# Kernel tuning notes

Measured on AMD Instinct MI355X. Metric: run time of the kernel, lower is better.

The kernel has to match this reference:

```python
import jax, jax.numpy as jnp
import numpy as np

N = 50000      # nodes
E = 800000     # edges (avg degree 16)
DIN = 256      # in_dim
EDIM = 16      # raw edge feature dim
H = 2          # heads
C = 64         # out_dim per head
NEG_SLOPE = 0.2


def setup_inputs() -> dict:
    key = jax.random.key(0)
    ks = jax.random.split(key, 10)
    s = 0.05
    return {
        "x": jax.random.normal(ks[0], (N, DIN), jnp.float32),
        "edge_index": jax.random.randint(ks[1], (2, E), 0, N, dtype=jnp.int64),
        "edge_attr": jax.random.normal(ks[2], (E, EDIM), jnp.float32),
        "W_ep": jax.random.normal(ks[3], (EDIM, DIN), jnp.float32) * s,
        "b_ep": jnp.zeros((DIN,), jnp.float32),
        "W_l": jax.random.normal(ks[4], (DIN, H * C), jnp.float32) * s,
        "b_l": jnp.zeros((H * C,), jnp.float32),
        "W_r": jax.random.normal(ks[5], (DIN, H * C), jnp.float32) * s,
        "b_r": jnp.zeros((H * C,), jnp.float32),
        "W_e": jax.random.normal(ks[6], (DIN, H * C), jnp.float32) * s,
        "att": jax.random.normal(ks[7], (H, C), jnp.float32) * s,
        "bias": jnp.zeros((H * C,), jnp.float32),
    }


def reference(x, edge_index, edge_attr, W_ep, b_ep, W_l, b_l, W_r, b_r, W_e, att, bias):
    src, dst = edge_index[0], edge_index[1]
    # edge_proj: Linear(edge_dim, in_dim)
    ea = edge_attr @ W_ep + b_ep                       # [E, DIN]
    # GATv2 node projections (lin_l -> source/message, lin_r -> target)
    xl = (x @ W_l + b_l).reshape(N, H, C)              # [N, H, C]
    xr = (x @ W_r + b_r).reshape(N, H, C)              # [N, H, C]
    ee = (ea @ W_e).reshape(E, H, C)                   # [E, H, C] (lin_edge, no bias)
    # per-edge combined features
    m = xl[src] + xr[dst] + ee                         # [E, H, C]
    # GATv2 attention score: att . LeakyReLU(m)
    s = jnp.einsum("ehc,hc->eh", jax.nn.leaky_relu(m, NEG_SLOPE), att)  # [E, H]
    # segment softmax over incoming edges of each target node
    smax = jax.ops.segment_max(s, dst, num_segments=N)  # [N, H]
    ex = jnp.exp(s - smax[dst])                         # [E, H]
    denom = jax.ops.segment_sum(ex, dst, num_segments=N)
    alpha = ex / denom[dst]                             # [E, H]
    # weighted scatter-add of source messages (xl[src])
    out = jax.ops.segment_sum(alpha[:, :, None] * xl[src], dst, num_segments=N)  # [N, H, C]
    return out.reshape(N, H * C) + bias
```

## Files before the change

### kernel.cpp

```cpp
#include <hip/hip_runtime.h>
#include <hip/hip_bf16.h>
#include <math.h>

#define DIN 256
#define EDIM 16
#define HC 128
#define GBM 64
#define GBN 256
#define GBK 32
#define LDS_STRIDE 40
#define BSTRIDE 64

typedef __attribute__((ext_vector_type(8))) short short8v;
typedef __attribute__((ext_vector_type(4))) float floatx4;
typedef __attribute__((ext_vector_type(2))) float floatx2;
typedef __attribute__((ext_vector_type(4))) unsigned short ushort4v;
typedef __attribute__((ext_vector_type(2))) int intx2;

__device__ inline unsigned short f2bf(float f) {
    union { float f; unsigned u; } v; v.f = f;
    unsigned r = v.u + 0x7FFF + ((v.u >> 16) & 1);
    return (unsigned short)(r >> 16);
}

__device__ inline float rsum32(float v) {
    int x;
    x = __builtin_amdgcn_update_dpp(0, __builtin_bit_cast(int, v), 0xB1, 0xF, 0xF, true);
    v += __builtin_bit_cast(float, x);
    x = __builtin_amdgcn_update_dpp(0, __builtin_bit_cast(int, v), 0x4E, 0xF, 0xF, true);
    v += __builtin_bit_cast(float, x);
    x = __builtin_amdgcn_update_dpp(0, __builtin_bit_cast(int, v), 0x124, 0xF, 0xF, true);
    v += __builtin_bit_cast(float, x);
    x = __builtin_amdgcn_update_dpp(0, __builtin_bit_cast(int, v), 0x128, 0xF, 0xF, true);
    v += __builtin_bit_cast(float, x);
    v += __builtin_bit_cast(float, __builtin_amdgcn_ds_swizzle(__builtin_bit_cast(int, v), 0x401F));
    return v;
}

__global__ void k_prep(const float* __restrict__ W_ep, const float* __restrict__ b_ep,
                       const float* __restrict__ W_e,
                       float* __restrict__ Wc, float* __restrict__ bc) {
    int tid = blockIdx.x * blockDim.x + threadIdx.x;
    if (tid < EDIM * HC) {
        int k = tid >> 7, j = tid & 127;
        float s = 0.f;
        for (int d = 0; d < DIN; ++d) s += W_ep[k * DIN + d] * W_e[d * HC + j];
        Wc[tid] = s;
    } else if (tid < EDIM * HC + HC) {
        int j = tid - EDIM * HC;
        float s = 0.f;
        for (int d = 0; d < DIN; ++d) s += b_ep[d] * W_e[d * HC + j];
        bc[j] = s;
    }
}

__global__ __launch_bounds__(256) void k_convw(const float* __restrict__ Wl,
                                               const float* __restrict__ Wr,
                                               unsigned short* __restrict__ Wb) {
    __shared__ unsigned short tile[32][33];
    int tx = threadIdx.x & 31, ty = threadIdx.x >> 5;
    int c0 = blockIdx.x * 32, k0 = blockIdx.y * 32;
#pragma unroll
    for (int i = 0; i < 4; ++i) {
        int k = k0 + ty + i * 8;
        int col = c0 + tx;
        float v = (col < HC) ? Wl[(size_t)k * HC + col] : Wr[(size_t)k * HC + (col - HC)];
        tile[ty + i * 8][tx] = f2bf(v);
    }
    __syncthreads();
#pragma unroll
    for (int i = 0; i < 4; ++i) {
        int col = c0 + ty + i * 8;
        int k = k0 + tx;
        Wb[(size_t)col * DIN + k] = tile[tx][ty + i * 8];
    }
}

__global__ __launch_bounds__(256) void k_mm(const float* __restrict__ x,
    const unsigned short* __restrict__ Wb,
    const float* __restrict__ bl, const float* __restrict__ br,
    unsigned* __restrict__ xlq, float* __restrict__ xrp, int M) {
    __shared__ unsigned short As[GBM * LDS_STRIDE];
    __shared__ unsigned short Bs[GBN * LDS_STRIDE];

    int t = threadIdx.x;
    int wid = t >> 6, lane = t & 63;
    int m0 = blockIdx.x * GBM;

    floatx4 acc[4][4];
#pragma unroll
    for (int i = 0; i < 4; ++i)
#pragma unroll
        for (int j = 0; j < 4; ++j) acc[i][j] = (floatx4){0.f, 0.f, 0.f, 0.f};

    int row_l = lane & 15, kg = (lane >> 4) * 8;

    for (int kb = 0; kb < DIN; kb += GBK) {
        {
            int r = t >> 2, kk = (t & 3) * 8;
            int gr = m0 + r; if (gr >= M) gr = M - 1;
            const float* xp = x + (size_t)gr * DIN + kb + kk;
            floatx4 v0 = *(const floatx4*)xp;
            floatx4 v1 = *(const floatx4*)(xp + 4);
            ushort4v u0, u1;
            u0[0] = f2bf(v0[0]); u0[1] = f2bf(v0[1]); u0[2] = f2bf(v0[2]); u0[3] = f2bf(v0[3]);
            u1[0] = f2bf(v1[0]); u1[1] = f2bf(v1[1]); u1[2] = f2bf(v1[2]); u1[3] = f2bf(v1[3]);
            *(ushort4v*)(&As[r * LDS_STRIDE + kk]) = u0;
            *(ushort4v*)(&As[r * LDS_STRIDE + kk + 4]) = u1;
        }
#pragma unroll
        for (int j = 0; j < 4; ++j) {
            int c = t + 256 * j;
            int col = c >> 2, kk = (c & 3) * 8;
            short8v v = *(const short8v*)(Wb + (size_t)col * DIN + kb + kk);
            *(short8v*)(&Bs[col * LDS_STRIDE + kk]) = v;
        }
        __syncthreads();

        short8v a[4], b[4];
#pragma unroll
        for (int i = 0; i < 4; ++i)
            a[i] = *(short8v*)(&As[(i * 16 + row_l) * LDS_STRIDE + kg]);
#pragma unroll
        for (int j = 0; j < 4; ++j)
            b[j] = *(short8v*)(&Bs[(wid * 64 + j * 16 + row_l) * LDS_STRIDE + kg]);
#pragma unroll
        for (int i = 0; i < 4; ++i)
#pragma unroll
            for (int j = 0; j < 4; ++j)
                acc[i][j] = __builtin_amdgcn_mfma_f32_16x16x32_bf16(a[i], b[j], acc[i][j], 0, 0, 0);
        __syncthreads();
    }

    int colf = lane & 15, rq = (lane >> 4) * 4;
    if (wid < 2) {
#pragma unroll
        for (int j = 0; j < 2; ++j) {
            int col = wid * 64 + j * 16 + colf;
            float bs_lo = bl[col], bs_hi = bl[col + 32];
            int l = wid * 32 + j * 16 + colf;
#pragma unroll
            for (int i = 0; i < 4; ++i) {
#pragma unroll
                for (int q = 0; q < 4; ++q) {
                    int row = m0 + i * 16 + rq + q;
                    if (row < M) {
                        unsigned lo = f2bf(acc[i][j][q] + bs_lo);
                        unsigned hi = f2bf(acc[i][j + 2][q] + bs_hi);
                        xlq[(size_t)row * 64 + l] = lo | (hi << 16);
                    }
                }
            }
        }
    } else {
#pragma unroll
        for (int j = 0; j < 4; ++j) {
            int col = wid * 64 + j * 16 + colf;
            int pc = col - HC;
            float bs = br[pc];
            int l = (pc >> 6) * 32 + (pc & 31);
            int slot = (pc >> 5) & 1;
#pragma unroll
            for (int i = 0; i < 4; ++i) {
#pragma unroll
                for (int q = 0; q < 4; ++q) {
                    int row = m0 + i * 16 + rq + q;
                    if (row < M) xrp[((size_t)row * 64 + l) * 2 + slot] = acc[i][j][q] + bs;
                }
            }
        }
    }
}

__global__ void k_scatter(const int* __restrict__ ei, int* __restrict__ cnt,
                          intx2* __restrict__ buckets, int E) {
    int e = blockIdx.x * blockDim.x + threadIdx.x;
    if (e < E) {
        int dst = ei[E + e];
        int pos = atomicAdd(&cnt[dst], 1);
        if (pos < BSTRIDE) {
            intx2 se; se.x = ei[e]; se.y = e;
            buckets[(size_t)dst * BSTRIDE + pos] = se;
        }
    }
}

__global__ __launch_bounds__(128, 4) void k_node(const unsigned* __restrict__ xlq,
    const float* __restrict__ xrp, const float* __restrict__ Wc,
    const float* __restrict__ bc, const float* __restrict__ att,
    const float* __restrict__ bias, const int* __restrict__ cnt,
    const intx2* __restrict__ buckets,
    const float* __restrict__ edge_attr, float* __restrict__ out, int n) {
    int wid = __builtin_amdgcn_readfirstlane(threadIdx.x >> 6);
    int lane = threadIdx.x & 63;
    int node = blockIdx.x * 2 + wid;
    if (node >= n) return;
    int g = lane >> 5;
    int ch_a = g * 64 + (lane & 31);
    int ch_b = ch_a + 32;

    floatx2 wc2[EDIM];
#pragma unroll
    for (int k = 0; k < EDIM; ++k) {
        wc2[k].x = Wc[k * HC + ch_a];
        wc2[k].y = Wc[k * HC + ch_b];
    }
    const float L2E = 1.44269504f;
    floatx2 att2; att2.x = att[ch_a] * L2E; att2.y = att[ch_b] * L2E;
    floatx2 xr2 = *(const floatx2*)(xrp + ((size_t)node * 64 + lane) * 2);
    floatx2 base2; base2.x = bc[ch_a] + xr2.x; base2.y = bc[ch_b] + xr2.y;

    int deg = cnt[node]; if (deg > BSTRIDE) deg = BSTRIDE;
    const intx2* __restrict__ bk = buckets + (size_t)node * BSTRIDE;

    int bsrc = 0, beid = 0;
    if (lane < deg) {
        intx2 se = bk[lane];
        bsrc = se.x; beid = se.y;
    }

    float D0 = 0.f, D1 = 0.f, D2 = 0.f, D3 = 0.f;
    floatx2 z; z.x = 0.f; z.y = 0.f;
    floatx2 acc0 = z, acc1 = z, acc2 = z, acc3 = z;

    for (int p = 0; p < deg; p += 4) {
        int s0 = __builtin_amdgcn_readlane(bsrc, p);
        int e0 = __builtin_amdgcn_readlane(beid, p);
        int s1 = __builtin_amdgcn_readlane(bsrc, p + 1);
        int e1 = __builtin_amdgcn_readlane(beid, p + 1);
        int s2 = __builtin_amdgcn_readlane(bsrc, p + 2);
        int e2 = __builtin_amdgcn_readlane(beid, p + 2);
        int s3 = __builtin_amdgcn_readlane(bsrc, p + 3);
        int e3 = __builtin_amdgcn_readlane(beid, p + 3);
        unsigned v0 = xlq[(size_t)s0 * 64 + lane];
        unsigned v1 = xlq[(size_t)s1 * 64 + lane];
        unsigned v2 = xlq[(size_t)s2 * 64 + lane];
        unsigned v3 = xlq[(size_t)s3 * 64 + lane];

#define SLOT(K, vv, ee_id, Dk, acck)                                              \
        {                                                                          \
            const floatx4* __restrict__ ea = (const floatx4*)(edge_attr + (size_t)(ee_id) * EDIM); \
            floatx2 ee = base2;                                                    \
            _Pragma("unroll")                                                      \
            for (int q = 0; q < 4; ++q) {                                          \
                floatx4 av = ea[q];                                                \
                _Pragma("unroll")                                                  \
                for (int k = 0; k < 4; ++k) ee += av[k] * wc2[q * 4 + k];          \
            }                                                                      \
            floatx2 xl2;                                                           \
            xl2.x = __builtin_bit_cast(float, (vv) << 16);                         \
            xl2.y = __builtin_bit_cast(float, (vv) & 0xFFFF0000u);                 \
            floatx2 m = xl2 + ee;                                                  \
            floatx2 lr;                                                            \
            lr.x = fmaxf(m.x, 0.f) + 0.2f * fminf(m.x, 0.f);                       \
            lr.y = fmaxf(m.y, 0.f) + 0.2f * fminf(m.y, 0.f);                       \
            float sc = lr.x * att2.x + lr.y * att2.y;                              \
            sc = rsum32(sc);                                                       \
            float w = (p + (K) < deg) ? exp2f(sc) : 0.f;                           \
            Dk += w;                                                               \
            acck += w * xl2;                                                       \
        }

        SLOT(0, v0, e0, D0, acc0)
        SLOT(1, v1, e1, D1, acc1)
        SLOT(2, v2, e2, D2, acc2)
        SLOT(3, v3, e3, D3, acc3)
#undef SLOT
    }

    float D = (D0 + D1) + (D2 + D3);
    floatx2 acc = (acc0 + acc1) + (acc2 + acc3);
    float invD = (D > 0.f) ? 1.f / D : 0.f;
    out[(size_t)node * HC + ch_a] = acc.x * invD + bias[ch_a];
    out[(size_t)node * HC + ch_b] = acc.y * invD + bias[ch_b];
}

extern "C" void kernel_launch(void* const* d_in, const int* in_sizes, int n_in,
                              void* d_out, int out_size, void* d_ws, size_t ws_size,
                              hipStream_t stream) {
    const float* x    = (const float*)d_in[0];
    const int*   ei   = (const int*)d_in[1];
    const float* eatt = (const float*)d_in[2];
    const float* W_ep = (const float*)d_in[3];
    const float* b_ep = (const float*)d_in[4];
    const float* W_l  = (const float*)d_in[5];
    const float* b_l  = (const float*)d_in[6];
    const float* W_r  = (const float*)d_in[7];
    const float* b_r  = (const float*)d_in[8];
    const float* W_e  = (const float*)d_in[9];
    const float* att  = (const float*)d_in[10];
    const float* bias = (const float*)d_in[11];
    float* out = (float*)d_out;

    const int N = in_sizes[0] / DIN;
    const int E = in_sizes[1] / 2;

    char* w = (char*)d_ws;
    size_t o = 0;
    auto alloc = [&](size_t bytes) {
        o = (o + 255) & ~(size_t)255;
        void* p = w + o;
        o += bytes;
        return p;
    };
    unsigned* xlq      = (unsigned*)alloc((size_t)N * 64 * sizeof(unsigned));
    float* xrp         = (float*)alloc((size_t)N * HC * sizeof(float));
    intx2* buckets     = (intx2*)alloc((size_t)N * BSTRIDE * sizeof(intx2));
    unsigned short* Wb = (unsigned short*)alloc((size_t)GBN * DIN * sizeof(unsigned short));
    float* Wc          = (float*)alloc(EDIM * HC * sizeof(float));
    float* bc          = (float*)alloc(HC * sizeof(float));
    int*   cnt         = (int*)alloc((size_t)N * sizeof(int));

    hipMemsetAsync(cnt, 0, (size_t)N * sizeof(int), stream);

    k_prep<<<(EDIM * HC + HC + 255) / 256, 256, 0, stream>>>(W_ep, b_ep, W_e, Wc, bc);
    {
        dim3 g(GBN / 32, DIN / 32);
        k_convw<<<g, 256, 0, stream>>>(W_l, W_r, Wb);
    }

    k_mm<<<(N + GBM - 1) / GBM, 256, 0, stream>>>(x, Wb, b_l, b_r, xlq, xrp, N);

    k_scatter<<<(E + 255) / 256, 256, 0, stream>>>(ei, cnt, buckets, E);

    k_node<<<(N + 1) / 2, 128, 0, stream>>>(xlq, xrp, Wc, bc, att, bias, cnt, buckets,
                                            eatt, out, N);
}
```

Measured before the change: 183.9 us.

## Merge setup kernels and memset; fuse edge scatter into GEMM launch

Folds the memset, weight-combine and weight-transpose kernels into one setup kernel. Also merges the edge bucket scatter and the node projection GEMM into one launch, with separate block ranges for each role so the two independent phases can run concurrently. This cuts launch overhead and lets the atomic-heavy scatter overlap with the matrix multiply. In exchange, scatter blocks and GEMM blocks compete for the same CUs, and the GEMM blocks keep their large LDS allocation even when a block only does scatter work.

```diff
diff --git a/kernel.cpp b/kernel.cpp
--- a/kernel.cpp
+++ b/kernel.cpp
@@ -37,55 +37,76 @@
     return v;
 }
 
-__global__ void k_prep(const float* __restrict__ W_ep, const float* __restrict__ b_ep,
-                       const float* __restrict__ W_e,
-                       float* __restrict__ Wc, float* __restrict__ bc) {
-    int tid = blockIdx.x * blockDim.x + threadIdx.x;
-    if (tid < EDIM * HC) {
-        int k = tid >> 7, j = tid & 127;
-        float s = 0.f;
-        for (int d = 0; d < DIN; ++d) s += W_ep[k * DIN + d] * W_e[d * HC + j];
-        Wc[tid] = s;
-    } else if (tid < EDIM * HC + HC) {
-        int j = tid - EDIM * HC;
-        float s = 0.f;
-        for (int d = 0; d < DIN; ++d) s += b_ep[d] * W_e[d * HC + j];
-        bc[j] = s;
-    }
-}
-
-__global__ __launch_bounds__(256) void k_convw(const float* __restrict__ Wl,
-                                               const float* __restrict__ Wr,
-                                               unsigned short* __restrict__ Wb) {
-    __shared__ unsigned short tile[32][33];
-    int tx = threadIdx.x & 31, ty = threadIdx.x >> 5;
-    int c0 = blockIdx.x * 32, k0 = blockIdx.y * 32;
-#pragma unroll
-    for (int i = 0; i < 4; ++i) {
-        int k = k0 + ty + i * 8;
-        int col = c0 + tx;
-        float v = (col < HC) ? Wl[(size_t)k * HC + col] : Wr[(size_t)k * HC + (col - HC)];
-        tile[ty + i * 8][tx] = f2bf(v);
-    }
-    __syncthreads();
-#pragma unroll
-    for (int i = 0; i < 4; ++i) {
-        int col = c0 + ty + i * 8;
-        int k = k0 + tx;
-        Wb[(size_t)col * DIN + k] = tile[tx][ty + i * 8];
-    }
-}
-
-__global__ __launch_bounds__(256) void k_mm(const float* __restrict__ x,
+__global__ __launch_bounds__(256) void k_setup(const float* __restrict__ W_ep,
+    const float* __restrict__ b_ep, const float* __restrict__ W_e,
+    const float* __restrict__ Wl, const float* __restrict__ Wr,
+    float* __restrict__ Wc, float* __restrict__ bc,
+    unsigned short* __restrict__ Wb, int* __restrict__ cnt, int n) {
+    const int NB_W = (GBN / 32) * (DIN / 32);
+    int b = blockIdx.x;
+    if (b < NB_W) {
+        __shared__ unsigned short tile[32][33];
+        int bx = b & 7, by = b >> 3;
+        int tx = threadIdx.x & 31, ty = threadIdx.x >> 5;
+        int c0 = bx * 32, k0 = by * 32;
+#pragma unroll
+        for (int i = 0; i < 4; ++i) {
+            int k = k0 + ty + i * 8;
+            int col = c0 + tx;
+            float v = (col < HC) ? Wl[(size_t)k * HC + col] : Wr[(size_t)k * HC + (col - HC)];
+            tile[ty + i * 8][tx] = f2bf(v);
+        }
+        __syncthreads();
+#pragma unroll
+        for (int i = 0; i < 4; ++i) {
+            int col = c0 + ty + i * 8;
+            int k = k0 + tx;
+            Wb[(size_t)col * DIN + k] = tile[tx][ty + i * 8];
+        }
+    } else if (b < NB_W + 9) {
+        int tid = (b - NB_W) * 256 + threadIdx.x;
+        if (tid < EDIM * HC) {
+            int k = tid >> 7, j = tid & 127;
+            float s = 0.f;
+            for (int d = 0; d < DIN; ++d) s += W_ep[k * DIN + d] * W_e[d * HC + j];
+            Wc[tid] = s;
+        } else if (tid < EDIM * HC + HC) {
+            int j = tid - EDIM * HC;
+            float s = 0.f;
+            for (int d = 0; d < DIN; ++d) s += b_ep[d] * W_e[d * HC + j];
+            bc[j] = s;
+        }
+    } else {
+        int i = (b - NB_W - 9) * 256 + threadIdx.x;
+        if (i < n) cnt[i] = 0;
+    }
+}
+
+__global__ __launch_bounds__(256) void k_mmsc(const float* __restrict__ x,
     const unsigned short* __restrict__ Wb,
     const float* __restrict__ bl, const float* __restrict__ br,
-    unsigned* __restrict__ xlq, float* __restrict__ xrp, int M) {
+    unsigned* __restrict__ xlq, float* __restrict__ xrp,
+    const int* __restrict__ ei, int* __restrict__ cnt,
+    intx2* __restrict__ buckets, int M, int E, int SCB) {
     __shared__ unsigned short As[GBM * LDS_STRIDE];
     __shared__ unsigned short Bs[GBN * LDS_STRIDE];
 
     int t = threadIdx.x;
+    if ((int)blockIdx.x < SCB) {
+        int e = blockIdx.x * 256 + t;
+        if (e < E) {
+            int dst = ei[E + e];
+            int pos = atomicAdd(&cnt[dst], 1);
+            if (pos < BSTRIDE) {
+                intx2 se; se.x = ei[e]; se.y = e;
+                buckets[(size_t)dst * BSTRIDE + pos] = se;
+            }
+        }
+        return;
+    }
+
     int wid = t >> 6, lane = t & 63;
-    int m0 = blockIdx.x * GBM;
+    int m0 = (blockIdx.x - SCB) * GBM;
 
     floatx4 acc[4][4];
 #pragma unroll
@@ -168,19 +189,6 @@
                     if (row < M) xrp[((size_t)row * 64 + l) * 2 + slot] = acc[i][j][q] + bs;
                 }
             }
-        }
-    }
-}
-
-__global__ void k_scatter(const int* __restrict__ ei, int* __restrict__ cnt,
-                          intx2* __restrict__ buckets, int E) {
-    int e = blockIdx.x * blockDim.x + threadIdx.x;
-    if (e < E) {
-        int dst = ei[E + e];
-        int pos = atomicAdd(&cnt[dst], 1);
-        if (pos < BSTRIDE) {
-            intx2 se; se.x = ei[e]; se.y = e;
-            buckets[(size_t)dst * BSTRIDE + pos] = se;
         }
     }
 }
@@ -311,17 +319,15 @@
     float* bc          = (float*)alloc(HC * sizeof(float));
     int*   cnt         = (int*)alloc((size_t)N * sizeof(int));
 
-    hipMemsetAsync(cnt, 0, (size_t)N * sizeof(int), stream);
-
-    k_prep<<<(EDIM * HC + HC + 255) / 256, 256, 0, stream>>>(W_ep, b_ep, W_e, Wc, bc);
-    {
-        dim3 g(GBN / 32, DIN / 32);
-        k_convw<<<g, 256, 0, stream>>>(W_l, W_r, Wb);
-    }
-
-    k_mm<<<(N + GBM - 1) / GBM, 256, 0, stream>>>(x, Wb, b_l, b_r, xlq, xrp, N);
-
-    k_scatter<<<(E + 255) / 256, 256, 0, stream>>>(ei, cnt, buckets, E);
+    const int NB_W = (GBN / 32) * (DIN / 32);
+    int setup_blocks = NB_W + 9 + (N + 255) / 256;
+    k_setup<<<setup_blocks, 256, 0, stream>>>(W_ep, b_ep, W_e, W_l, W_r,
+                                              Wc, bc, Wb, cnt, N);
+
+    int SCB = (E + 255) / 256;
+    int MMB = (N + GBM - 1) / GBM;
+    k_mmsc<<<SCB + MMB, 256, 0, stream>>>(x, Wb, b_l, b_r, xlq, xrp,
+                                          ei, cnt, buckets, N, E, SCB);
 
     k_node<<<(N + 1) / 2, 128, 0, stream>>>(xlq, xrp, Wc, bc, att, bias, cnt, buckets,
                                             eatt, out, N);
```

After: 194.2 us. 5.6% more time.
